# Kernel tuning notes

Hardware: AMD Instinct MI355X
Metric: run time of the kernel (lower is better)

Reference implementation:

```python
import jax, jax.numpy as jnp
import numpy as np

N_STEPS = 20      # max(n_steps_al, n_steps_kc)
ALPHA   = 0.9     # membrane decay exp(-dt/tau_m)
V_TH    = 1.0     # spiking threshold
G_SOMA  = 0.3     # dendrite->axon coupling conductance (2-compartment KC)
APL_GAIN = 1.0    # graded APL gain
I_SCALE = 0.5     # graded ORN drive scale
BETA    = 10.0    # surrogate-gradient sharpness ('soft' sigmoid)

@jax.custom_vjp
def spike(x):
    return (x > 0).astype(x.dtype)

def _spike_fwd(x):
    return spike(x), x

def _spike_bwd(x, g):
    s = jax.nn.sigmoid(BETA * x)
    return (g * BETA * s * (1.0 - s),)

spike.defvjp(_spike_fwd, _spike_bwd)


def _sparse_w(key, shape, density):
    k1, k2 = jax.random.split(key)
    mask = jax.random.bernoulli(k1, density, shape)
    w = jax.random.uniform(k2, shape)
    return (mask * w).astype(jnp.float32)


def setup_inputs() -> dict:
    key = jax.random.key(0)
    ks = jax.random.split(key, 10)
    batch, n_or, n_orn, n_ln, n_pn, n_kc, n_odors = 4096, 21, 42, 56, 42, 2000, 34
    or_input = jax.random.uniform(ks[0], (batch, n_or), dtype=jnp.float32)
    or_gains = jnp.ones((n_or,), jnp.float32)
    # fixed OR->ORN mapping: OR i drives left (2i) and right (2i+1) ORNs
    m = np.zeros((n_or, n_orn), np.float32)
    for i in range(n_or):
        m[i, 2 * i] = 1.0
        m[i, 2 * i + 1] = 1.0
    mapping = jnp.asarray(m)
    orn_to_pn = _sparse_w(ks[1], (n_orn, n_pn), 0.3)
    orn_to_ln = _sparse_w(ks[2], (n_orn, n_ln), 0.3)
    ln_to_pn = _sparse_w(ks[3], (n_ln, n_pn), 0.3)
    pn_to_kc = _sparse_w(ks[4], (n_pn, n_kc), 0.15)  # ~6 PN claws per KC
    kc_to_apl = jax.random.uniform(ks[5], (n_kc, 1), dtype=jnp.float32) * 0.01
    apl_to_kc = jax.random.uniform(ks[6], (1, n_kc), dtype=jnp.float32)
    dec_w = jax.random.normal(ks[7], (n_kc, n_odors), dtype=jnp.float32) * 0.02
    dec_b = jnp.zeros((n_odors,), jnp.float32)
    return {"or_input": or_input, "or_gains": or_gains, "mapping": mapping,
            "orn_to_pn": orn_to_pn, "orn_to_ln": orn_to_ln, "ln_to_pn": ln_to_pn,
            "pn_to_kc": pn_to_kc, "kc_to_apl": kc_to_apl, "apl_to_kc": apl_to_kc,
            "dec_w": dec_w, "dec_b": dec_b}


def reference(or_input, or_gains, mapping, orn_to_pn, orn_to_ln, ln_to_pn,
              pn_to_kc, kc_to_apl, apl_to_kc, dec_w, dec_b):
    B = or_input.shape[0]
    n_orn, n_pn = orn_to_pn.shape
    n_ln = orn_to_ln.shape[1]
    n_kc = pn_to_kc.shape[1]
    # OR transduction: graded, learnable per-OR gain
    orn_drive = (or_input * jax.nn.softplus(or_gains)) @ mapping  # [B, n_orn]

    z = lambda n: jnp.zeros((B, n), or_input.dtype)
    carry0 = (z(n_orn), z(n_ln), z(n_pn), z(n_kc), z(n_kc), z(1), z(n_kc))

    def step(carry, _):
        v_orn, v_ln, v_pn, v_d, v_a, apl, kc_cnt = carry
        # ORN LIF driven by graded OR current
        v_orn = ALPHA * v_orn + I_SCALE * orn_drive
        s_orn = spike(v_orn - V_TH)
        v_orn = v_orn * (1.0 - s_orn)
        # LN LIF (lateral inhibition interneurons)
        v_ln = ALPHA * v_ln + s_orn @ orn_to_ln
        s_ln = spike(v_ln - V_TH)
        v_ln = v_ln * (1.0 - s_ln)
        # PN LIF: ORN excitation, LN inhibition
        v_pn = ALPHA * v_pn + s_orn @ orn_to_pn - s_ln @ ln_to_pn
        s_pn = spike(v_pn - V_TH)
        v_pn = v_pn * (1.0 - s_pn)
        # KC 2-compartment: dendrite gets PN input and APL inhibition
        v_d = ALPHA * v_d + s_pn @ pn_to_kc - apl @ apl_to_kc
        v_a = ALPHA * v_a + G_SOMA * (v_d - v_a)
        s_kc = spike(v_a - V_TH)
        v_a = v_a * (1.0 - s_kc)
        # APL: graded (non-spiking) global inhibition from KC spikes
        apl = APL_GAIN * jax.nn.relu(s_kc @ kc_to_apl)
        return (v_orn, v_ln, v_pn, v_d, v_a, apl, kc_cnt + s_kc), None

    carry, _ = jax.lax.scan(step, carry0, None, length=N_STEPS)
    kc_count = carry[-1]
    kc_rates = kc_count / N_STEPS
    logits = kc_rates @ dec_w + dec_b  # [B, n_odors]
    return logits
```

## Files before the change

kernel.cpp:

```cpp
#include <hip/hip_runtime.h>

#define NSTEPS 20
#define ALPHA  0.9f
#define VTH    1.0f
#define GSOMA  0.3f
#define ISCALE 0.5f

#define NOR  21
#define NORN 42
#define NLN  56
#define NPN  42
#define NKC  2000
#define NOD  34

#define TPB  256
#define KPER 8

__global__ __launch_bounds__(TPB)
void phase1_kernel(const float* __restrict__ or_input,
                   const float* __restrict__ or_gains,
                   const float* __restrict__ mapping,
                   const float* __restrict__ orn_to_pn,
                   const float* __restrict__ orn_to_ln,
                   const float* __restrict__ ln_to_pn,
                   unsigned long long* __restrict__ g_masks,
                   int batch)
{
    __shared__ float sW_ol[NORN * NLN + 24];
    __shared__ float sW_op[NORN * NPN + 24];
    __shared__ float sW_lp[NLN * NPN + 24];
    __shared__ float sSpg[NOR];

    const int tid  = threadIdx.x;
    const int lane = tid & 63;
    const int wid  = tid >> 6;

    for (int i = tid; i < NORN * NLN; i += TPB) sW_ol[i] = orn_to_ln[i];
    for (int i = tid; i < NORN * NPN; i += TPB) sW_op[i] = orn_to_pn[i];
    for (int i = tid; i < NLN * NPN;  i += TPB) sW_lp[i] = ln_to_pn[i];
    if (tid < NOR) sSpg[tid] = log1pf(expf(or_gains[tid]));
    __syncthreads();

    const int row = blockIdx.x * 4 + wid;
    if (row >= batch) return;

    float drive = 0.f;
    if (lane < NORN) {
        const float* x = or_input + (long)row * NOR;
        for (int i = 0; i < NOR; ++i) drive += x[i] * sSpg[i] * mapping[i * NORN + lane];
        drive *= ISCALE;
    }

    float v_orn = 0.f, v_ln = 0.f, v_pn = 0.f;
    unsigned long long* outm = g_masks + (long)row * NSTEPS;

    for (int t = 0; t < NSTEPS; ++t) {
        bool so = false;
        if (lane < NORN) {
            v_orn = ALPHA * v_orn + drive;
            so = (v_orn - VTH) > 0.f;
            if (so) v_orn = 0.f;
        }
        const unsigned long long mOrn = __ballot(so);

        float aln = 0.f, apn = 0.f;
        {
            unsigned long long m = mOrn;
            while (m) {
                int o0 = __builtin_ctzll(m); m &= m - 1;
                int o1 = o0, o2 = o0, o3 = o0;
                float f1 = 0.f, f2 = 0.f, f3 = 0.f;
                if (m) { o1 = __builtin_ctzll(m); m &= m - 1; f1 = 1.f; }
                if (m) { o2 = __builtin_ctzll(m); m &= m - 1; f2 = 1.f; }
                if (m) { o3 = __builtin_ctzll(m); m &= m - 1; f3 = 1.f; }
                float l0 = sW_ol[o0 * NLN + lane];
                float l1 = sW_ol[o1 * NLN + lane];
                float l2 = sW_ol[o2 * NLN + lane];
                float l3 = sW_ol[o3 * NLN + lane];
                float p0 = sW_op[o0 * NPN + lane];
                float p1 = sW_op[o1 * NPN + lane];
                float p2 = sW_op[o2 * NPN + lane];
                float p3 = sW_op[o3 * NPN + lane];
                aln += l0; aln += f1 * l1; aln += f2 * l2; aln += f3 * l3;
                apn += p0; apn += f1 * p1; apn += f2 * p2; apn += f3 * p3;
            }
        }

        bool sl = false;
        if (lane < NLN) {
            v_ln = ALPHA * v_ln + aln;
            sl = (v_ln - VTH) > 0.f;
            if (sl) v_ln = 0.f;
        }
        const unsigned long long mLn = __ballot(sl);

        float h = 0.f;
        {
            unsigned long long m = mLn;
            while (m) {
                int l0i = __builtin_ctzll(m); m &= m - 1;
                int l1i = l0i, l2i = l0i, l3i = l0i;
                float f1 = 0.f, f2 = 0.f, f3 = 0.f;
                if (m) { l1i = __builtin_ctzll(m); m &= m - 1; f1 = 1.f; }
                if (m) { l2i = __builtin_ctzll(m); m &= m - 1; f2 = 1.f; }
                if (m) { l3i = __builtin_ctzll(m); m &= m - 1; f3 = 1.f; }
                float w0 = sW_lp[l0i * NPN + lane];
                float w1 = sW_lp[l1i * NPN + lane];
                float w2 = sW_lp[l2i * NPN + lane];
                float w3 = sW_lp[l3i * NPN + lane];
                h += w0; h += f1 * w1; h += f2 * w2; h += f3 * w3;
            }
        }

        bool sp = false;
        if (lane < NPN) {
            v_pn = ALPHA * v_pn + apn - h;
            sp = (v_pn - VTH) > 0.f;
            if (sp) v_pn = 0.f;
        }
        const unsigned long long mPn = __ballot(sp);
        if (lane == 0) outm[t] = mPn;
    }
}

__global__ __launch_bounds__(TPB)
void phase2_kernel(const unsigned long long* __restrict__ g_masks,
                   const float* __restrict__ pn_to_kc,
                   const float* __restrict__ kc_to_apl,
                   const float* __restrict__ apl_to_kc,
                   const float* __restrict__ dec_w,
                   const float* __restrict__ dec_b,
                   float* __restrict__ out)
{
    __shared__ float sRed[2][4];
    __shared__ float sRed2[4 * NOD];

    const int tid  = threadIdx.x;
    const int lane = tid & 63;
    const int wid  = tid >> 6;
    const int b    = blockIdx.x;

    const int  kbase = tid * KPER;
    const bool act   = (kbase < NKC);
    float vd[KPER], va[KPER], cnt[KPER], wa2k[KPER], wk2a[KPER];
#pragma unroll
    for (int j = 0; j < KPER; ++j) { vd[j] = 0.f; va[j] = 0.f; cnt[j] = 0.f; }
    {
        const float4* a4 = (const float4*)(apl_to_kc + (act ? kbase : 0));
        const float4* k4 = (const float4*)(kc_to_apl + (act ? kbase : 0));
        float4 a0 = a4[0], a1 = a4[1], k0 = k4[0], k1 = k4[1];
        const float g = act ? 1.f : 0.f;
        wa2k[0] = g * a0.x; wa2k[1] = g * a0.y; wa2k[2] = g * a0.z; wa2k[3] = g * a0.w;
        wa2k[4] = g * a1.x; wa2k[5] = g * a1.y; wa2k[6] = g * a1.z; wa2k[7] = g * a1.w;
        wk2a[0] = g * k0.x; wk2a[1] = g * k0.y; wk2a[2] = g * k0.z; wk2a[3] = g * k0.w;
        wk2a[4] = g * k1.x; wk2a[5] = g * k1.y; wk2a[6] = g * k1.z; wk2a[7] = g * k1.w;
    }
    if (tid < 8) sRed[tid >> 2][tid & 3] = 0.f;
    __syncthreads();

    const unsigned long long* gm = g_masks + (long)b * NSTEPS;

    for (int t = 0; t < NSTEPS; ++t) {
        const float* rp = sRed[(t + 1) & 1];
        const float apl = fmaxf(rp[0] + rp[1] + rp[2] + rp[3], 0.f);

#pragma unroll
        for (int j = 0; j < KPER; ++j) vd[j] = ALPHA * vd[j] - apl * wa2k[j];

        unsigned long long m = gm[t];
        while (m) {
            const int p0 = __builtin_ctzll(m); m &= m - 1;
            int p1 = p0; float f1 = 0.f;
            if (m) { p1 = __builtin_ctzll(m); m &= m - 1; f1 = 1.f; }
            if (act) {
                const float4* w0 = (const float4*)(pn_to_kc + (long)p0 * NKC + kbase);
                const float4* w1 = (const float4*)(pn_to_kc + (long)p1 * NKC + kbase);
                float4 a0 = w0[0], a1 = w0[1];
                float4 b0 = w1[0], b1 = w1[1];
                vd[0] += a0.x; vd[1] += a0.y; vd[2] += a0.z; vd[3] += a0.w;
                vd[4] += a1.x; vd[5] += a1.y; vd[6] += a1.z; vd[7] += a1.w;
                vd[0] += f1 * b0.x; vd[1] += f1 * b0.y; vd[2] += f1 * b0.z; vd[3] += f1 * b0.w;
                vd[4] += f1 * b1.x; vd[5] += f1 * b1.y; vd[6] += f1 * b1.z; vd[7] += f1 * b1.w;
            }
        }

        float aplp = 0.f;
#pragma unroll
        for (int j = 0; j < KPER; ++j) {
            va[j] = ALPHA * va[j] + GSOMA * (vd[j] - va[j]);
            float s = (va[j] - VTH) > 0.f ? 1.f : 0.f;
            va[j] *= (1.f - s);
            cnt[j] += s;
            aplp += s * wk2a[j];
        }
        for (int off = 32; off > 0; off >>= 1) aplp += __shfl_xor(aplp, off, 64);
        if (lane == 0) sRed[t & 1][wid] = aplp;
        __syncthreads();
    }

    float acc[NOD];
#pragma unroll
    for (int o = 0; o < NOD; ++o) acc[o] = 0.f;
    if (act) {
#pragma unroll
        for (int j = 0; j < KPER; ++j) {
            float r = cnt[j] / 20.0f;
            if (r != 0.f) {
                const float* wr = dec_w + (long)(kbase + j) * NOD;
#pragma unroll
                for (int o = 0; o < NOD; ++o) acc[o] += r * wr[o];
            }
        }
    }
#pragma unroll
    for (int o = 0; o < NOD; ++o) {
        float v = acc[o];
        for (int off = 32; off > 0; off >>= 1) v += __shfl_xor(v, off, 64);
        if (lane == 0) sRed2[wid * NOD + o] = v;
    }
    __syncthreads();
    if (tid < NOD) {
        float v = sRed2[tid] + sRed2[NOD + tid] + sRed2[2 * NOD + tid] +
                  sRed2[3 * NOD + tid] + dec_b[tid];
        out[(long)b * NOD + tid] = v;
    }
}

__global__ __launch_bounds__(TPB)
void snn_fused(const float* __restrict__ or_input, const float* __restrict__ or_gains,
               const float* __restrict__ mapping, const float* __restrict__ orn_to_pn,
               const float* __restrict__ orn_to_ln, const float* __restrict__ ln_to_pn,
               const float* __restrict__ pn_to_kc, const float* __restrict__ kc_to_apl,
               const float* __restrict__ apl_to_kc, const float* __restrict__ dec_w,
               const float* __restrict__ dec_b, float* __restrict__ out)
{
    __shared__ float sW_ol[NORN * NLN];
    __shared__ float sW_op[NORN * NPN];
    __shared__ float sW_lp[NLN * NPN];
    __shared__ float sDrive[NORN];
    __shared__ float sSpg[NOR];
    __shared__ float sOrn[NORN];
    __shared__ float sLn[NLN];
    __shared__ float sApl;
    __shared__ float sRed[4];
    __shared__ float sRed2[4 * NOD];
    __shared__ unsigned long long sMask;

    const int tid = threadIdx.x;
    const int b   = blockIdx.x;

    for (int i = tid; i < NORN * NLN; i += TPB) sW_ol[i] = orn_to_ln[i];
    for (int i = tid; i < NORN * NPN; i += TPB) sW_op[i] = orn_to_pn[i];
    for (int i = tid; i < NLN * NPN;  i += TPB) sW_lp[i] = ln_to_pn[i];
    if (tid < NOR) sSpg[tid] = log1pf(expf(or_gains[tid]));
    if (tid == 0)  sApl = 0.f;
    __syncthreads();

    if (tid < NORN) {
        const float* x = or_input + (long)b * NOR;
        float d = 0.f;
        for (int i = 0; i < NOR; ++i) d += x[i] * sSpg[i] * mapping[i * NORN + tid];
        sDrive[tid] = d * ISCALE;
    }

    const int  kbase = tid * KPER;
    const bool act   = (kbase < NKC);
    float vd[KPER], va[KPER], cnt[KPER], wa2k[KPER], wk2a[KPER];
#pragma unroll
    for (int j = 0; j < KPER; ++j) {
        vd[j] = 0.f; va[j] = 0.f; cnt[j] = 0.f;
        wa2k[j] = act ? apl_to_kc[kbase + j] : 0.f;
        wk2a[j] = act ? kc_to_apl[kbase + j] : 0.f;
    }
    float v_orn = 0.f, v_ln = 0.f, v_pn = 0.f, v_pn_exc = 0.f;
    __syncthreads();

    for (int t = 0; t < NSTEPS; ++t) {
        if (tid < NORN) {
            v_orn = ALPHA * v_orn + sDrive[tid];
            float s = (v_orn - VTH) > 0.f ? 1.f : 0.f;
            v_orn *= (1.f - s);
            sOrn[tid] = s;
        }
        __syncthreads();
        if (tid < NLN) {
            float a = 0.f;
            for (int o = 0; o < NORN; ++o) a += sOrn[o] * sW_ol[o * NLN + tid];
            v_ln = ALPHA * v_ln + a;
            float s = (v_ln - VTH) > 0.f ? 1.f : 0.f;
            v_ln *= (1.f - s);
            sLn[tid] = s;
        } else if (tid >= 64 && tid < 64 + NPN) {
            const int j = tid - 64;
            float a = 0.f;
            for (int o = 0; o < NORN; ++o) a += sOrn[o] * sW_op[o * NPN + j];
            v_pn_exc = a;
        }
        __syncthreads();
        if (tid >= 64 && tid < 64 + NPN) {
            const int j = tid - 64;
            float inh = 0.f;
            for (int l = 0; l < NLN; ++l) inh += sLn[l] * sW_lp[l * NPN + j];
            v_pn = ALPHA * v_pn + v_pn_exc - inh;
            bool s = (v_pn - VTH) > 0.f;
            if (s) v_pn = 0.f;
            unsigned long long bal = __ballot(s);
            if (tid == 64) sMask = bal;
        }
        __syncthreads();
        {
            const float apl = sApl;
#pragma unroll
            for (int j = 0; j < KPER; ++j) vd[j] = ALPHA * vd[j] - apl * wa2k[j];
            unsigned long long m = sMask;
            while (m) {
                const int p = __builtin_ctzll(m);
                m &= m - 1;
                if (act) {
                    const float4* w = (const float4*)(pn_to_kc + (long)p * NKC + kbase);
                    float4 w0 = w[0], w1 = w[1];
                    vd[0] += w0.x; vd[1] += w0.y; vd[2] += w0.z; vd[3] += w0.w;
                    vd[4] += w1.x; vd[5] += w1.y; vd[6] += w1.z; vd[7] += w1.w;
                }
            }
            float aplp = 0.f;
#pragma unroll
            for (int j = 0; j < KPER; ++j) {
                va[j] = ALPHA * va[j] + GSOMA * (vd[j] - va[j]);
                float s = (va[j] - VTH) > 0.f ? 1.f : 0.f;
                va[j] *= (1.f - s);
                cnt[j] += s;
                aplp += s * wk2a[j];
            }
            for (int off = 32; off > 0; off >>= 1) aplp += __shfl_xor(aplp, off, 64);
            if ((tid & 63) == 0) sRed[tid >> 6] = aplp;
        }
        __syncthreads();
        if (tid == 0) {
            float a = sRed[0] + sRed[1] + sRed[2] + sRed[3];
            sApl = fmaxf(a, 0.f);
        }
    }

    float acc[NOD];
#pragma unroll
    for (int o = 0; o < NOD; ++o) acc[o] = 0.f;
    if (act) {
#pragma unroll
        for (int j = 0; j < KPER; ++j) {
            float r = cnt[j] / 20.0f;
            if (r != 0.f) {
                const float* wr = dec_w + (long)(kbase + j) * NOD;
#pragma unroll
                for (int o = 0; o < NOD; ++o) acc[o] += r * wr[o];
            }
        }
    }
#pragma unroll
    for (int o = 0; o < NOD; ++o) {
        float v = acc[o];
        for (int off = 32; off > 0; off >>= 1) v += __shfl_xor(v, off, 64);
        if ((tid & 63) == 0) sRed2[(tid >> 6) * NOD + o] = v;
    }
    __syncthreads();
    if (tid < NOD) {
        float v = sRed2[tid] + sRed2[NOD + tid] + sRed2[2 * NOD + tid] +
                  sRed2[3 * NOD + tid] + dec_b[tid];
        out[(long)b * NOD + tid] = v;
    }
}

extern "C" void kernel_launch(void* const* d_in, const int* in_sizes, int n_in,
                              void* d_out, int out_size, void* d_ws, size_t ws_size,
                              hipStream_t stream) {
    (void)n_in; (void)out_size;
    const float* or_input  = (const float*)d_in[0];
    const float* or_gains  = (const float*)d_in[1];
    const float* mapping   = (const float*)d_in[2];
    const float* orn_to_pn = (const float*)d_in[3];
    const float* orn_to_ln = (const float*)d_in[4];
    const float* ln_to_pn  = (const float*)d_in[5];
    const float* pn_to_kc  = (const float*)d_in[6];
    const float* kc_to_apl = (const float*)d_in[7];
    const float* apl_to_kc = (const float*)d_in[8];
    const float* dec_w     = (const float*)d_in[9];
    const float* dec_b     = (const float*)d_in[10];
    float* out = (float*)d_out;

    const int batch = in_sizes[0] / NOR;
    const size_t need = (size_t)batch * NSTEPS * sizeof(unsigned long long);

    if (ws_size >= need) {
        unsigned long long* g_masks = (unsigned long long*)d_ws;
        hipLaunchKernelGGL(phase1_kernel, dim3((batch + 3) / 4), dim3(TPB), 0, stream,
                           or_input, or_gains, mapping, orn_to_pn, orn_to_ln, ln_to_pn,
                           g_masks, batch);
        hipLaunchKernelGGL(phase2_kernel, dim3(batch), dim3(TPB), 0, stream,
                           g_masks, pn_to_kc, kc_to_apl, apl_to_kc, dec_w, dec_b, out);
    } else {
        hipLaunchKernelGGL(snn_fused, dim3(batch), dim3(TPB), 0, stream,
                           or_input, or_gains, mapping, orn_to_pn, orn_to_ln,
                           ln_to_pn, pn_to_kc, kc_to_apl, apl_to_kc, dec_w, dec_b, out);
    }
}
```

Before: 237.1 us.

## Hold phase-1 antennal-lobe weights in registers and use dense shuffle matvecs

Phase 1 becomes a one-wavefront-per-row kernel that loads each lane's column of the ORN->LN, ORN->PN and LN->PN weights into registers instead of LDS. The sparse ballot/ctz spike-index loops are replaced by fully unrolled dense loops that broadcast spikes with __shfl and accumulate multiply-adds. This removes LDS traffic and divergent index loops, but every lane now does all 42/56 FMAs per step, each block reloads about 140 weights from global memory, and register pressure goes up.

```diff
diff --git a/kernel.cpp b/kernel.cpp
--- a/kernel.cpp
+++ b/kernel.cpp
@@ -16,38 +16,44 @@
 #define TPB  256
 #define KPER 8
 
-__global__ __launch_bounds__(TPB)
-void phase1_kernel(const float* __restrict__ or_input,
-                   const float* __restrict__ or_gains,
-                   const float* __restrict__ mapping,
-                   const float* __restrict__ orn_to_pn,
-                   const float* __restrict__ orn_to_ln,
-                   const float* __restrict__ ln_to_pn,
-                   unsigned long long* __restrict__ g_masks,
-                   int batch)
+__global__ __launch_bounds__(64, 2)
+void phase1_reg(const float* __restrict__ or_input,
+                const float* __restrict__ or_gains,
+                const float* __restrict__ mapping,
+                const float* __restrict__ orn_to_pn,
+                const float* __restrict__ orn_to_ln,
+                const float* __restrict__ ln_to_pn,
+                unsigned long long* __restrict__ g_masks,
+                int batch)
 {
-    __shared__ float sW_ol[NORN * NLN + 24];
-    __shared__ float sW_op[NORN * NPN + 24];
-    __shared__ float sW_lp[NLN * NPN + 24];
-    __shared__ float sSpg[NOR];
-
-    const int tid  = threadIdx.x;
-    const int lane = tid & 63;
-    const int wid  = tid >> 6;
-
-    for (int i = tid; i < NORN * NLN; i += TPB) sW_ol[i] = orn_to_ln[i];
-    for (int i = tid; i < NORN * NPN; i += TPB) sW_op[i] = orn_to_pn[i];
-    for (int i = tid; i < NLN * NPN;  i += TPB) sW_lp[i] = ln_to_pn[i];
-    if (tid < NOR) sSpg[tid] = log1pf(expf(or_gains[tid]));
-    __syncthreads();
-
-    const int row = blockIdx.x * 4 + wid;
+    const int lane = threadIdx.x;
+    const int row  = blockIdx.x;
     if (row >= batch) return;
 
+    const int jl = lane < NLN ? lane : 0;
+    const int jp = lane < NPN ? lane : 0;
+
+    float wOl[NORN], wOp[NORN], wLp[NLN];
+#pragma unroll
+    for (int o = 0; o < NORN; ++o) {
+        wOl[o] = orn_to_ln[o * NLN + jl];
+        wOp[o] = orn_to_pn[o * NPN + jp];
+    }
+#pragma unroll
+    for (int l = 0; l < NLN; ++l) wLp[l] = ln_to_pn[l * NPN + jp];
+
+    float spg = 0.f;
+    if (lane < NOR) spg = log1pf(expf(or_gains[lane]));
+
     float drive = 0.f;
-    if (lane < NORN) {
+    {
         const float* x = or_input + (long)row * NOR;
-        for (int i = 0; i < NOR; ++i) drive += x[i] * sSpg[i] * mapping[i * NORN + lane];
+        const int jo = lane < NORN ? lane : 0;
+#pragma unroll
+        for (int i = 0; i < NOR; ++i) {
+            float g = __shfl(spg, i);
+            drive += x[i] * g * mapping[i * NORN + jo];
+        }
         drive *= ISCALE;
     }
 
@@ -55,61 +61,31 @@
     unsigned long long* outm = g_masks + (long)row * NSTEPS;
 
     for (int t = 0; t < NSTEPS; ++t) {
-        bool so = false;
+        float so = 0.f;
         if (lane < NORN) {
             v_orn = ALPHA * v_orn + drive;
-            so = (v_orn - VTH) > 0.f;
-            if (so) v_orn = 0.f;
-        }
-        const unsigned long long mOrn = __ballot(so);
+            if (v_orn - VTH > 0.f) { so = 1.f; v_orn = 0.f; }
+        }
 
         float aln = 0.f, apn = 0.f;
-        {
-            unsigned long long m = mOrn;
-            while (m) {
-                int o0 = __builtin_ctzll(m); m &= m - 1;
-                int o1 = o0, o2 = o0, o3 = o0;
-                float f1 = 0.f, f2 = 0.f, f3 = 0.f;
-                if (m) { o1 = __builtin_ctzll(m); m &= m - 1; f1 = 1.f; }
-                if (m) { o2 = __builtin_ctzll(m); m &= m - 1; f2 = 1.f; }
-                if (m) { o3 = __builtin_ctzll(m); m &= m - 1; f3 = 1.f; }
-                float l0 = sW_ol[o0 * NLN + lane];
-                float l1 = sW_ol[o1 * NLN + lane];
-                float l2 = sW_ol[o2 * NLN + lane];
-                float l3 = sW_ol[o3 * NLN + lane];
-                float p0 = sW_op[o0 * NPN + lane];
-                float p1 = sW_op[o1 * NPN + lane];
-                float p2 = sW_op[o2 * NPN + lane];
-                float p3 = sW_op[o3 * NPN + lane];
-                aln += l0; aln += f1 * l1; aln += f2 * l2; aln += f3 * l3;
-                apn += p0; apn += f1 * p1; apn += f2 * p2; apn += f3 * p3;
-            }
-        }
-
-        bool sl = false;
+#pragma unroll
+        for (int o = 0; o < NORN; ++o) {
+            float s = __shfl(so, o);
+            aln += s * wOl[o];
+            apn += s * wOp[o];
+        }
+
+        float sl = 0.f;
         if (lane < NLN) {
             v_ln = ALPHA * v_ln + aln;
-            sl = (v_ln - VTH) > 0.f;
-            if (sl) v_ln = 0.f;
-        }
-        const unsigned long long mLn = __ballot(sl);
+            if (v_ln - VTH > 0.f) { sl = 1.f; v_ln = 0.f; }
+        }
 
         float h = 0.f;
-        {
-            unsigned long long m = mLn;
-            while (m) {
-                int l0i = __builtin_ctzll(m); m &= m - 1;
-                int l1i = l0i, l2i = l0i, l3i = l0i;
-                float f1 = 0.f, f2 = 0.f, f3 = 0.f;
-                if (m) { l1i = __builtin_ctzll(m); m &= m - 1; f1 = 1.f; }
-                if (m) { l2i = __builtin_ctzll(m); m &= m - 1; f2 = 1.f; }
-                if (m) { l3i = __builtin_ctzll(m); m &= m - 1; f3 = 1.f; }
-                float w0 = sW_lp[l0i * NPN + lane];
-                float w1 = sW_lp[l1i * NPN + lane];
-                float w2 = sW_lp[l2i * NPN + lane];
-                float w3 = sW_lp[l3i * NPN + lane];
-                h += w0; h += f1 * w1; h += f2 * w2; h += f3 * w3;
-            }
+#pragma unroll
+        for (int l = 0; l < NLN; ++l) {
+            float s = __shfl(sl, l);
+            h += s * wLp[l];
         }
 
         bool sp = false;
@@ -392,7 +368,7 @@
 
     if (ws_size >= need) {
         unsigned long long* g_masks = (unsigned long long*)d_ws;
-        hipLaunchKernelGGL(phase1_kernel, dim3((batch + 3) / 4), dim3(TPB), 0, stream,
+        hipLaunchKernelGGL(phase1_reg, dim3(batch), dim3(64), 0, stream,
                            or_input, or_gains, mapping, orn_to_pn, orn_to_ln, ln_to_pn,
                            g_masks, batch);
         hipLaunchKernelGGL(phase2_kernel, dim3(batch), dim3(TPB), 0, stream,
```

Result: slower. 336.7 us (+42.0%).

## Split phase1 into ORN/LN and PN kernels with register-resident weights

Applied to the files above, without the earlier changes.

The antennal-lobe stage now runs as two kernels instead of one. The first computes ORN and LN spike masks per batch row. The second computes PN masks from those masks, holding its weights in per-lane registers and doing branch-free bitmask dot products instead of shared-memory ctz loops. Each uses one 64-thread block per row. This removes the per-block shared-memory weight staging and the data-dependent loop in phase1, at the cost of an extra launch, extra workspace traffic and higher register pressure.

```diff
diff --git a/kernel.cpp b/kernel.cpp
--- a/kernel.cpp
+++ b/kernel.cpp
@@ -16,15 +16,234 @@
 #define TPB  256
 #define KPER 8
 
+__global__ __launch_bounds__(64)
+void phase1a(const float* __restrict__ or_input,
+             const float* __restrict__ or_gains,
+             const float* __restrict__ mapping,
+             const float* __restrict__ orn_to_ln,
+             ulonglong2* __restrict__ gAB,
+             int batch)
+{
+    const int lane = threadIdx.x;
+    const int row  = blockIdx.x;
+    if (row >= batch) return;
+
+    const int jl = lane < NLN ? lane : 0;
+    float wOl[NORN];
+#pragma unroll
+    for (int o = 0; o < NORN; ++o) wOl[o] = orn_to_ln[o * NLN + jl];
+
+    float spg = 0.f;
+    if (lane < NOR) spg = log1pf(expf(or_gains[lane]));
+
+    float drive = 0.f;
+    {
+        const float* x = or_input + (long)row * NOR;
+        const int jo = lane < NORN ? lane : 0;
+#pragma unroll
+        for (int i = 0; i < NOR; ++i) {
+            float g = __shfl(spg, i);
+            drive += x[i] * g * mapping[i * NORN + jo];
+        }
+        drive *= ISCALE;
+    }
+
+    float v_orn = 0.f, v_ln = 0.f;
+    ulonglong2* outm = gAB + (long)row * NSTEPS;
+
+    for (int t = 0; t < NSTEPS; ++t) {
+        bool so = false;
+        if (lane < NORN) {
+            v_orn = ALPHA * v_orn + drive;
+            so = (v_orn - VTH) > 0.f;
+            if (so) v_orn = 0.f;
+        }
+        const unsigned long long mOrn = __ballot(so);
+        const unsigned int mo_lo = (unsigned int)mOrn;
+        const unsigned int mo_hi = (unsigned int)(mOrn >> 32);
+
+        float aln = 0.f;
+#pragma unroll
+        for (int o = 0; o < 32; ++o) aln += (float)((mo_lo >> o) & 1u) * wOl[o];
+#pragma unroll
+        for (int o = 32; o < NORN; ++o) aln += (float)((mo_hi >> (o - 32)) & 1u) * wOl[o];
+
+        bool sl = false;
+        if (lane < NLN) {
+            v_ln = ALPHA * v_ln + aln;
+            sl = (v_ln - VTH) > 0.f;
+            if (sl) v_ln = 0.f;
+        }
+        const unsigned long long mLn = __ballot(sl);
+        if (lane == 0) outm[t] = make_ulonglong2(mOrn, mLn);
+    }
+}
+
+__global__ __launch_bounds__(64)
+void phase1b(const float* __restrict__ orn_to_pn,
+             const float* __restrict__ ln_to_pn,
+             const ulonglong2* __restrict__ gAB,
+             unsigned long long* __restrict__ gPN,
+             int batch)
+{
+    const int lane = threadIdx.x;
+    const int row  = blockIdx.x;
+    if (row >= batch) return;
+
+    const int jp = lane < NPN ? lane : 0;
+    float wOp[NORN], wLp[NLN];
+#pragma unroll
+    for (int o = 0; o < NORN; ++o) wOp[o] = orn_to_pn[o * NPN + jp];
+#pragma unroll
+    for (int l = 0; l < NLN; ++l) wLp[l] = ln_to_pn[l * NPN + jp];
+
+    const ulonglong2* inm = gAB + (long)row * NSTEPS;
+    unsigned long long* outm = gPN + (long)row * NSTEPS;
+
+    float v_pn = 0.f;
+    ulonglong2 ab = inm[0];
+
+    for (int t = 0; t < NSTEPS; ++t) {
+        ulonglong2 abn;
+        if (t < NSTEPS - 1) abn = inm[t + 1];
+
+        const unsigned int mo_lo = (unsigned int)ab.x;
+        const unsigned int mo_hi = (unsigned int)(ab.x >> 32);
+        const unsigned int ml_lo = (unsigned int)ab.y;
+        const unsigned int ml_hi = (unsigned int)(ab.y >> 32);
+
+        float apn = 0.f;
+#pragma unroll
+        for (int o = 0; o < 32; ++o) apn += (float)((mo_lo >> o) & 1u) * wOp[o];
+#pragma unroll
+        for (int o = 32; o < NORN; ++o) apn += (float)((mo_hi >> (o - 32)) & 1u) * wOp[o];
+
+        float h = 0.f;
+#pragma unroll
+        for (int l = 0; l < 32; ++l) h += (float)((ml_lo >> l) & 1u) * wLp[l];
+#pragma unroll
+        for (int l = 32; l < NLN; ++l) h += (float)((ml_hi >> (l - 32)) & 1u) * wLp[l];
+
+        bool sp = false;
+        if (lane < NPN) {
+            v_pn = ALPHA * v_pn + apn - h;
+            sp = (v_pn - VTH) > 0.f;
+            if (sp) v_pn = 0.f;
+        }
+        const unsigned long long mPn = __ballot(sp);
+        if (lane == 0) outm[t] = mPn;
+        ab = abn;
+    }
+}
+
 __global__ __launch_bounds__(TPB)
-void phase1_kernel(const float* __restrict__ or_input,
-                   const float* __restrict__ or_gains,
-                   const float* __restrict__ mapping,
-                   const float* __restrict__ orn_to_pn,
-                   const float* __restrict__ orn_to_ln,
-                   const float* __restrict__ ln_to_pn,
-                   unsigned long long* __restrict__ g_masks,
-                   int batch)
+void phase2_kernel(const unsigned long long* __restrict__ g_masks,
+                   const float* __restrict__ pn_to_kc,
+                   const float* __restrict__ kc_to_apl,
+                   const float* __restrict__ apl_to_kc,
+                   const float* __restrict__ dec_w,
+                   const float* __restrict__ dec_b,
+                   float* __restrict__ out)
+{
+    __shared__ float sRed[2][4];
+    __shared__ float sRed2[4 * NOD];
+
+    const int tid  = threadIdx.x;
+    const int lane = tid & 63;
+    const int wid  = tid >> 6;
+    const int b    = blockIdx.x;
+
+    const int  kbase = tid * KPER;
+    const bool act   = (kbase < NKC);
+    float vd[KPER], va[KPER], cnt[KPER], wa2k[KPER], wk2a[KPER];
+#pragma unroll
+    for (int j = 0; j < KPER; ++j) { vd[j] = 0.f; va[j] = 0.f; cnt[j] = 0.f; }
+    {
+        const float4* a4 = (const float4*)(apl_to_kc + (act ? kbase : 0));
+        const float4* k4 = (const float4*)(kc_to_apl + (act ? kbase : 0));
+        float4 a0 = a4[0], a1 = a4[1], k0 = k4[0], k1 = k4[1];
+        const float g = act ? 1.f : 0.f;
+        wa2k[0] = g * a0.x; wa2k[1] = g * a0.y; wa2k[2] = g * a0.z; wa2k[3] = g * a0.w;
+        wa2k[4] = g * a1.x; wa2k[5] = g * a1.y; wa2k[6] = g * a1.z; wa2k[7] = g * a1.w;
+        wk2a[0] = g * k0.x; wk2a[1] = g * k0.y; wk2a[2] = g * k0.z; wk2a[3] = g * k0.w;
+        wk2a[4] = g * k1.x; wk2a[5] = g * k1.y; wk2a[6] = g * k1.z; wk2a[7] = g * k1.w;
+    }
+    if (tid < 8) sRed[tid >> 2][tid & 3] = 0.f;
+    __syncthreads();
+
+    const unsigned long long* gm = g_masks + (long)b * NSTEPS;
+
+    for (int t = 0; t < NSTEPS; ++t) {
+        const float* rp = sRed[(t + 1) & 1];
+        const float apl = fmaxf(rp[0] + rp[1] + rp[2] + rp[3], 0.f);
+
+#pragma unroll
+        for (int j = 0; j < KPER; ++j) vd[j] = ALPHA * vd[j] - apl * wa2k[j];
+
+        unsigned long long m = gm[t];
+        while (m) {
+            const int p0 = __builtin_ctzll(m); m &= m - 1;
+            int p1 = p0; float f1 = 0.f;
+            if (m) { p1 = __builtin_ctzll(m); m &= m - 1; f1 = 1.f; }
+            if (act) {
+                const float4* w0 = (const float4*)(pn_to_kc + (long)p0 * NKC + kbase);
+                const float4* w1 = (const float4*)(pn_to_kc + (long)p1 * NKC + kbase);
+                float4 a0 = w0[0], a1 = w0[1];
+                float4 b0 = w1[0], b1 = w1[1];
+                vd[0] += a0.x; vd[1] += a0.y; vd[2] += a0.z; vd[3] += a0.w;
+                vd[4] += a1.x; vd[5] += a1.y; vd[6] += a1.z; vd[7] += a1.w;
+                vd[0] += f1 * b0.x; vd[1] += f1 * b0.y; vd[2] += f1 * b0.z; vd[3] += f1 * b0.w;
+                vd[4] += f1 * b1.x; vd[5] += f1 * b1.y; vd[6] += f1 * b1.z; vd[7] += f1 * b1.w;
+            }
+        }
+
+        float aplp = 0.f;
+#pragma unroll
+        for (int j = 0; j < KPER; ++j) {
+            va[j] = ALPHA * va[j] + GSOMA * (vd[j] - va[j]);
+            float s = (va[j] - VTH) > 0.f ? 1.f : 0.f;
+            va[j] *= (1.f - s);
+            cnt[j] += s;
+            aplp += s * wk2a[j];
+        }
+        for (int off = 32; off > 0; off >>= 1) aplp += __shfl_xor(aplp, off, 64);
+        if (lane == 0) sRed[t & 1][wid] = aplp;
+        __syncthreads();
+    }
+
+    float acc[NOD];
+#pragma unroll
+    for (int o = 0; o < NOD; ++o) acc[o] = 0.f;
+    if (act) {
+#pragma unroll
+        for (int j = 0; j < KPER; ++j) {
+            float r = cnt[j] / 20.0f;
+            if (r != 0.f) {
+                const float* wr = dec_w + (long)(kbase + j) * NOD;
+#pragma unroll
+                for (int o = 0; o < NOD; ++o) acc[o] += r * wr[o];
+            }
+        }
+    }
+#pragma unroll
+    for (int o = 0; o < NOD; ++o) {
+        float v = acc[o];
+        for (int off = 32; off > 0; off >>= 1) v += __shfl_xor(v, off, 64);
+        if (lane == 0) sRed2[wid * NOD + o] = v;
+    }
+    __syncthreads();
+    if (tid < NOD) {
+        float v = sRed2[tid] + sRed2[NOD + tid] + sRed2[2 * NOD + tid] +
+                  sRed2[3 * NOD + tid] + dec_b[tid];
+        out[(long)b * NOD + tid] = v;
+    }
+}
+
+__global__ __launch_bounds__(TPB)
+void phase1_ctz(const float* __restrict__ or_input, const float* __restrict__ or_gains,
+                const float* __restrict__ mapping, const float* __restrict__ orn_to_pn,
+                const float* __restrict__ orn_to_ln, const float* __restrict__ ln_to_pn,
+                unsigned long long* __restrict__ g_masks, int batch)
 {
     __shared__ float sW_ol[NORN * NLN + 24];
     __shared__ float sW_op[NORN * NPN + 24];
@@ -124,109 +343,6 @@
 }
 
 __global__ __launch_bounds__(TPB)
-void phase2_kernel(const unsigned long long* __restrict__ g_masks,
-                   const float* __restrict__ pn_to_kc,
-                   const float* __restrict__ kc_to_apl,
-                   const float* __restrict__ apl_to_kc,
-                   const float* __restrict__ dec_w,
-                   const float* __restrict__ dec_b,
-                   float* __restrict__ out)
-{
-    __shared__ float sRed[2][4];
-    __shared__ float sRed2[4 * NOD];
-
-    const int tid  = threadIdx.x;
-    const int lane = tid & 63;
-    const int wid  = tid >> 6;
-    const int b    = blockIdx.x;
-
-    const int  kbase = tid * KPER;
-    const bool act   = (kbase < NKC);
-    float vd[KPER], va[KPER], cnt[KPER], wa2k[KPER], wk2a[KPER];
-#pragma unroll
-    for (int j = 0; j < KPER; ++j) { vd[j] = 0.f; va[j] = 0.f; cnt[j] = 0.f; }
-    {
-        const float4* a4 = (const float4*)(apl_to_kc + (act ? kbase : 0));
-        const float4* k4 = (const float4*)(kc_to_apl + (act ? kbase : 0));
-        float4 a0 = a4[0], a1 = a4[1], k0 = k4[0], k1 = k4[1];
-        const float g = act ? 1.f : 0.f;
-        wa2k[0] = g * a0.x; wa2k[1] = g * a0.y; wa2k[2] = g * a0.z; wa2k[3] = g * a0.w;
-        wa2k[4] = g * a1.x; wa2k[5] = g * a1.y; wa2k[6] = g * a1.z; wa2k[7] = g * a1.w;
-        wk2a[0] = g * k0.x; wk2a[1] = g * k0.y; wk2a[2] = g * k0.z; wk2a[3] = g * k0.w;
-        wk2a[4] = g * k1.x; wk2a[5] = g * k1.y; wk2a[6] = g * k1.z; wk2a[7] = g * k1.w;
-    }
-    if (tid < 8) sRed[tid >> 2][tid & 3] = 0.f;
-    __syncthreads();
-
-    const unsigned long long* gm = g_masks + (long)b * NSTEPS;
-
-    for (int t = 0; t < NSTEPS; ++t) {
-        const float* rp = sRed[(t + 1) & 1];
-        const float apl = fmaxf(rp[0] + rp[1] + rp[2] + rp[3], 0.f);
-
-#pragma unroll
-        for (int j = 0; j < KPER; ++j) vd[j] = ALPHA * vd[j] - apl * wa2k[j];
-
-        unsigned long long m = gm[t];
-        while (m) {
-            const int p0 = __builtin_ctzll(m); m &= m - 1;
-            int p1 = p0; float f1 = 0.f;
-            if (m) { p1 = __builtin_ctzll(m); m &= m - 1; f1 = 1.f; }
-            if (act) {
-                const float4* w0 = (const float4*)(pn_to_kc + (long)p0 * NKC + kbase);
-                const float4* w1 = (const float4*)(pn_to_kc + (long)p1 * NKC + kbase);
-                float4 a0 = w0[0], a1 = w0[1];
-                float4 b0 = w1[0], b1 = w1[1];
-                vd[0] += a0.x; vd[1] += a0.y; vd[2] += a0.z; vd[3] += a0.w;
-                vd[4] += a1.x; vd[5] += a1.y; vd[6] += a1.z; vd[7] += a1.w;
-                vd[0] += f1 * b0.x; vd[1] += f1 * b0.y; vd[2] += f1 * b0.z; vd[3] += f1 * b0.w;
-                vd[4] += f1 * b1.x; vd[5] += f1 * b1.y; vd[6] += f1 * b1.z; vd[7] += f1 * b1.w;
-            }
-        }
-
-        float aplp = 0.f;
-#pragma unroll
-        for (int j = 0; j < KPER; ++j) {
-            va[j] = ALPHA * va[j] + GSOMA * (vd[j] - va[j]);
-            float s = (va[j] - VTH) > 0.f ? 1.f : 0.f;
-            va[j] *= (1.f - s);
-            cnt[j] += s;
-            aplp += s * wk2a[j];
-        }
-        for (int off = 32; off > 0; off >>= 1) aplp += __shfl_xor(aplp, off, 64);
-        if (lane == 0) sRed[t & 1][wid] = aplp;
-        __syncthreads();
-    }
-
-    float acc[NOD];
-#pragma unroll
-    for (int o = 0; o < NOD; ++o) acc[o] = 0.f;
-    if (act) {
-#pragma unroll
-        for (int j = 0; j < KPER; ++j) {
-            float r = cnt[j] / 20.0f;
-            if (r != 0.f) {
-                const float* wr = dec_w + (long)(kbase + j) * NOD;
-#pragma unroll
-                for (int o = 0; o < NOD; ++o) acc[o] += r * wr[o];
-            }
-        }
-    }
-#pragma unroll
-    for (int o = 0; o < NOD; ++o) {
-        float v = acc[o];
-        for (int off = 32; off > 0; off >>= 1) v += __shfl_xor(v, off, 64);
-        if (lane == 0) sRed2[wid * NOD + o] = v;
-    }
-    __syncthreads();
-    if (tid < NOD) {
-        float v = sRed2[tid] + sRed2[NOD + tid] + sRed2[2 * NOD + tid] +
-                  sRed2[3 * NOD + tid] + dec_b[tid];
-        out[(long)b * NOD + tid] = v;
-    }
-}
-
-__global__ __launch_bounds__(TPB)
 void snn_fused(const float* __restrict__ or_input, const float* __restrict__ or_gains,
                const float* __restrict__ mapping, const float* __restrict__ orn_to_pn,
                const float* __restrict__ orn_to_ln, const float* __restrict__ ln_to_pn,
@@ -388,15 +504,25 @@
     float* out = (float*)d_out;
 
     const int batch = in_sizes[0] / NOR;
-    const size_t need = (size_t)batch * NSTEPS * sizeof(unsigned long long);
-
-    if (ws_size >= need) {
-        unsigned long long* g_masks = (unsigned long long*)d_ws;
-        hipLaunchKernelGGL(phase1_kernel, dim3((batch + 3) / 4), dim3(TPB), 0, stream,
+    const size_t needAB = (size_t)batch * NSTEPS * sizeof(ulonglong2);
+    const size_t needPN = (size_t)batch * NSTEPS * sizeof(unsigned long long);
+
+    if (ws_size >= needAB + needPN) {
+        ulonglong2* gAB = (ulonglong2*)d_ws;
+        unsigned long long* gPN = (unsigned long long*)((char*)d_ws + needAB);
+        hipLaunchKernelGGL(phase1a, dim3(batch), dim3(64), 0, stream,
+                           or_input, or_gains, mapping, orn_to_ln, gAB, batch);
+        hipLaunchKernelGGL(phase1b, dim3(batch), dim3(64), 0, stream,
+                           orn_to_pn, ln_to_pn, gAB, gPN, batch);
+        hipLaunchKernelGGL(phase2_kernel, dim3(batch), dim3(TPB), 0, stream,
+                           gPN, pn_to_kc, kc_to_apl, apl_to_kc, dec_w, dec_b, out);
+    } else if (ws_size >= needPN) {
+        unsigned long long* gPN = (unsigned long long*)d_ws;
+        hipLaunchKernelGGL(phase1_ctz, dim3((batch + 3) / 4), dim3(TPB), 0, stream,
                            or_input, or_gains, mapping, orn_to_pn, orn_to_ln, ln_to_pn,
-                           g_masks, batch);
+                           gPN, batch);
         hipLaunchKernelGGL(phase2_kernel, dim3(batch), dim3(TPB), 0, stream,
-                           g_masks, pn_to_kc, kc_to_apl, apl_to_kc, dec_w, dec_b, out);
+                           gPN, pn_to_kc, kc_to_apl, apl_to_kc, dec_w, dec_b, out);
     } else {
         hipLaunchKernelGGL(snn_fused, dim3(batch), dim3(TPB), 0, stream,
                            or_input, or_gains, mapping, orn_to_pn, orn_to_ln,
```

New measurement: 210.7 us. 11.1% less time.
